# Kernel tuning notes

Measured on AMD Instinct MI355X. Metric: run time of the kernel, lower is better.

## Reference

```python
import jax, jax.numpy as jnp
import numpy as np

N_NODES = 50000
N_EDGES = 800000
IN_F = 512
H_F = 32
HEADS = 8
N_CLS = 40
NEG_SLOPE = 0.2


def gat_conv(h, W, al, ar, b, src, dst, n_heads, d_out):
    """DGL-style GATConv. h: [N, F_in]; W: [F_in, n_heads*d_out];
    al, ar: [n_heads, d_out]; b: [n_heads*d_out]. Returns [N, n_heads, d_out]."""
    n = h.shape[0]
    feat = (h @ W).reshape(n, n_heads, d_out)            # [N, H, D]
    el = jnp.sum(feat * al[None], axis=-1)               # [N, H]
    er = jnp.sum(feat * ar[None], axis=-1)               # [N, H]
    e = jax.nn.leaky_relu(el[src] + er[dst], NEG_SLOPE)  # [E, H]
    # numerically stable edge softmax per destination node
    m = jax.ops.segment_max(e, dst, num_segments=n)      # [N, H]
    m = jnp.where(jnp.isfinite(m), m, 0.0)
    ee = jnp.exp(e - m[dst])                             # [E, H]
    den = jax.ops.segment_sum(ee, dst, num_segments=n)   # [N, H]
    alpha = ee / jnp.maximum(den[dst], 1e-9)             # [E, H]
    msg = alpha[:, :, None] * feat[src]                  # [E, H, D]
    rst = jax.ops.segment_sum(msg, dst, num_segments=n)  # [N, H, D]
    return rst + b.reshape(1, n_heads, d_out)


def setup_inputs() -> dict:
    key = jax.random.key(0)
    ks = jax.random.split(key, 16)
    hid = H_F * HEADS
    s = lambda fan: 1.0 / np.sqrt(fan)
    return {
        "in_feat": jax.random.normal(ks[0], (N_NODES, IN_F), jnp.float32),
        "src": jax.random.randint(ks[1], (N_EDGES,), 0, N_NODES, jnp.int32),
        "dst": jax.random.randint(ks[2], (N_EDGES,), 0, N_NODES, jnp.int32),
        "W0": jax.random.normal(ks[3], (IN_F, hid), jnp.float32) * s(IN_F),
        "al0": jax.random.normal(ks[4], (HEADS, H_F), jnp.float32) * s(H_F),
        "ar0": jax.random.normal(ks[5], (HEADS, H_F), jnp.float32) * s(H_F),
        "b0": jnp.zeros((hid,), jnp.float32),
        "W1": jax.random.normal(ks[6], (hid, hid), jnp.float32) * s(hid),
        "al1": jax.random.normal(ks[7], (HEADS, H_F), jnp.float32) * s(H_F),
        "ar1": jax.random.normal(ks[8], (HEADS, H_F), jnp.float32) * s(H_F),
        "b1": jnp.zeros((hid,), jnp.float32),
        "W2": jax.random.normal(ks[9], (hid, N_CLS), jnp.float32) * s(hid),
        "al2": jax.random.normal(ks[10], (1, N_CLS), jnp.float32) * s(N_CLS),
        "ar2": jax.random.normal(ks[11], (1, N_CLS), jnp.float32) * s(N_CLS),
        "b2": jnp.zeros((N_CLS,), jnp.float32),
    }


def reference(in_feat, src, dst, W0, al0, ar0, b0, W1, al1, ar1, b1,
              W2, al2, ar2, b2):
    n = in_feat.shape[0]
    # layer 0 + ReLU (dropout p=0.0 is identity) + flatten heads
    h = gat_conv(in_feat, W0, al0, ar0, b0, src, dst, HEADS, H_F)
    h = jax.nn.relu(h).reshape(n, -1)
    # layer 1
    h = gat_conv(h, W1, al1, ar1, b1, src, dst, HEADS, H_F)
    h = jax.nn.relu(h).reshape(n, -1)
    # output layer, single head, no activation
    h = gat_conv(h, W2, al2, ar2, b2, src, dst, 1, N_CLS)
    return h.reshape(n, -1)
```

## Files before the change

kernel.cpp:

```cpp
#include <hip/hip_runtime.h>
#include <hip/hip_bf16.h>

#define N_NODES 50000
#define N_EDGES 800000
#define IN_F 512
#define HID 256
#define HEADS 8
#define DHEAD 32
#define N_CLS 40
#define NCLS_PAD 64

typedef __bf16 bf16x8 __attribute__((ext_vector_type(8)));
typedef float f32x4 __attribute__((ext_vector_type(4)));
typedef float f32x2 __attribute__((ext_vector_type(2)));

#define AT_AL0 0
#define AT_AR0 256
#define AT_AL1 512
#define AT_AR1 768
#define AT_AL2 1024
#define AT_AR2 1088
#define AT_B0  1152
#define AT_B1  1408
#define AT_B2  1664
#define AT_SZ  1792

__device__ __forceinline__ float ldflag(const void* p, long long i, int isbf) {
  return isbf ? __bfloat162float(((const __hip_bfloat16*)p)[i])
              : ((const float*)p)[i];
}
__device__ __forceinline__ float blo(unsigned u) { return __uint_as_float(u << 16); }
__device__ __forceinline__ float bhi(unsigned u) { return __uint_as_float(u & 0xffff0000u); }
__device__ __forceinline__ f32x2 bpair(unsigned u) {
  f32x2 r;
  r.x = __uint_as_float(u << 16);
  r.y = __uint_as_float(u & 0xffff0000u);
  return r;
}
__device__ __forceinline__ unsigned pk2(float a, float b) {
  unsigned x = __bfloat16_as_ushort(__float2bfloat16(a));
  unsigned y = __bfloat16_as_ushort(__float2bfloat16(b));
  return x | (y << 16);
}
__device__ __forceinline__ void gload16(const unsigned short* g, unsigned short* l) {
  __builtin_amdgcn_global_load_lds((__attribute__((address_space(1))) void*)g,
                                   (__attribute__((address_space(3))) void*)l, 16, 0, 0);
}

__global__ void k_detect_prep(const unsigned short* __restrict__ raw, int* __restrict__ flag,
                              const void* al0, const void* ar0, const void* al1, const void* ar1,
                              const void* al2, const void* ar2, const void* b0, const void* b1,
                              const void* b2, float* __restrict__ att, int* __restrict__ cursor) {
  __shared__ int cnt[256];
  int t = threadIdx.x;
  for (int i = t; i < N_NODES; i += 256) cursor[i] = 0;
  int c = 0;
  for (int i = t; i < 8192; i += 256) {
    int e = (raw[i] >> 7) & 0xFF;
    if (e >= 0x90) c++;
  }
  cnt[t] = c;
  __syncthreads();
  for (int s = 128; s; s >>= 1) {
    if (t < s) cnt[t] += cnt[t + s];
    __syncthreads();
  }
  __shared__ int sflag;
  if (t == 0) { sflag = (cnt[0] > 64) ? 0 : 1; *flag = sflag; }
  __syncthreads();
  int isbf = sflag;
  att[AT_AL0 + t] = ldflag(al0, t, isbf);
  att[AT_AR0 + t] = ldflag(ar0, t, isbf);
  att[AT_AL1 + t] = ldflag(al1, t, isbf);
  att[AT_AR1 + t] = ldflag(ar1, t, isbf);
  att[AT_B0 + t]  = ldflag(b0, t, isbf);
  att[AT_B1 + t]  = ldflag(b1, t, isbf);
  if (t < N_CLS) {
    att[AT_AL2 + t] = ldflag(al2, t, isbf);
    att[AT_AR2 + t] = ldflag(ar2, t, isbf);
    att[AT_B2 + t]  = ldflag(b2, t, isbf);
  }
}

__global__ void k_hist(const int* __restrict__ dst, int* __restrict__ cnt) {
  int e = blockIdx.x * blockDim.x + threadIdx.x;
  if (e < N_EDGES) atomicAdd(&cnt[dst[e]], 1);
}

#define SCAN_B 512
#define SCAN_NB ((N_NODES + SCAN_B - 1) / SCAN_B)

__global__ __launch_bounds__(SCAN_B) void k_scan_blocks(const int* __restrict__ deg,
                                                        int* __restrict__ excl,
                                                        int* __restrict__ partial) {
  __shared__ int buf[SCAN_B];
  int t = threadIdx.x;
  int i = blockIdx.x * SCAN_B + t;
  int v = (i < N_NODES) ? deg[i] : 0;
  buf[t] = v;
  __syncthreads();
  for (int off = 1; off < SCAN_B; off <<= 1) {
    int x = (t >= off) ? buf[t - off] : 0;
    __syncthreads();
    buf[t] += x;
    __syncthreads();
  }
  if (i < N_NODES) excl[i] = buf[t] - v;
  if (t == SCAN_B - 1) partial[blockIdx.x] = buf[t];
}

__global__ void k_scan_partials(int* __restrict__ partial, int* __restrict__ rowptr) {
  __shared__ int buf[SCAN_NB];
  int t = threadIdx.x;
  if (t < SCAN_NB) buf[t] = partial[t];
  __syncthreads();
  if (t == 0) {
    int run = 0;
    for (int b = 0; b < SCAN_NB; b++) { int v = buf[b]; buf[b] = run; run += v; }
    rowptr[N_NODES] = run;
  }
  __syncthreads();
  if (t < SCAN_NB) partial[t] = buf[t];
}

__global__ void k_scan_add(int* __restrict__ rowptr, const int* __restrict__ partial,
                           int* __restrict__ cursor) {
  int i = blockIdx.x * blockDim.x + threadIdx.x;
  if (i < N_NODES) {
    rowptr[i] += partial[i / SCAN_B];
    cursor[i] = 0;
  }
}

__global__ void k_scatter(const int* __restrict__ src, const int* __restrict__ dst,
                          const int* __restrict__ rowptr, int* __restrict__ cursor,
                          int* __restrict__ csr_src) {
  int e = blockIdx.x * blockDim.x + threadIdx.x;
  if (e < N_EDGES) {
    int d = dst[e];
    int pos = rowptr[d] + atomicAdd(&cursor[d], 1);
    csr_src[pos] = src[e];
  }
}

#define TW0 (HID * IN_F)
#define TW1 (TW0 + HID * HID)
#define TW2 (TW1 + NCLS_PAD * HID)
__global__ void k_transpose_all(const void* __restrict__ W0, const void* __restrict__ W1,
                                const void* __restrict__ W2,
                                __hip_bfloat16* __restrict__ w0t, __hip_bfloat16* __restrict__ w1t,
                                __hip_bfloat16* __restrict__ w2t, const int* __restrict__ flag) {
  int isbf = *flag;
  int i = blockIdx.x * blockDim.x + threadIdx.x;
  if (i < TW0) {
    int n = i >> 9, k = i & 511;
    w0t[i] = __float2bfloat16(ldflag(W0, (long long)k * HID + n, isbf));
  } else if (i < TW1) {
    int j = i - TW0;
    int n = j >> 8, k = j & 255;
    w1t[j] = __float2bfloat16(ldflag(W1, (long long)k * HID + n, isbf));
  } else if (i < TW2) {
    int j = i - TW1;
    int n = j >> 8, k = j & 255;
    float v = (n < N_CLS) ? ldflag(W2, (long long)k * N_CLS + n, isbf) : 0.f;
    w2t[j] = __float2bfloat16(v);
  }
}

__device__ __forceinline__ uint4 loadA(const void* A, int isbf, int ga, int M, int K, int off) {
  uint4 av = make_uint4(0u, 0u, 0u, 0u);
  if (ga < M) {
    if (isbf) {
      av = *(const uint4*)((const __hip_bfloat16*)A + (size_t)ga * K + off);
    } else {
      const float* ap = (const float*)A + (size_t)ga * K + off;
      float4 f1 = *(const float4*)ap;
      float4 f2 = *(const float4*)(ap + 4);
      av.x = pk2(f1.x, f1.y); av.y = pk2(f1.z, f1.w);
      av.z = pk2(f2.x, f2.y); av.w = pk2(f2.z, f2.w);
    }
  }
  return av;
}

__global__ __launch_bounds__(256) void k_gemm128(const void* __restrict__ A,
                                                 const __hip_bfloat16* __restrict__ Bt,
                                                 __hip_bfloat16* __restrict__ C,
                                                 int M, int K, int N,
                                                 const int* __restrict__ flag, int force_bf,
                                                 const float* __restrict__ al,
                                                 const float* __restrict__ ar,
                                                 float* __restrict__ el,
                                                 float* __restrict__ er, int fuse_eler) {
  __shared__ unsigned short sA[128 * 32];
  __shared__ unsigned short sB[128 * 32];
  const int isbf = force_bf ? 1 : *flag;
  int nwg = gridDim.x;
  int q = nwg >> 3, r = nwg & 7;
  int xcd = blockIdx.x & 7, lid = blockIdx.x >> 3;
  int logical = (xcd < r ? xcd * (q + 1) : r * (q + 1) + (xcd - r) * q) + lid;
  int nblk = N >> 7;
  int mb = logical / nblk;
  int nb = logical - mb * nblk;
  int m0 = mb * 128, n0 = nb * 128;
  int tid = threadIdx.x;
  int wave = tid >> 6, lane = tid & 63;
  int wm = (wave >> 1) * 64, wn = (wave & 1) * 64;
  int lm = lane & 15, quad = lane >> 4;
  int c0 = (wave << 7) + lane, c1 = c0 + 64;
  int rA0 = c0 >> 2, rA1 = c1 >> 2;
  int col0 = (c0 & 3) << 3, col1 = (c1 & 3) << 3;
  int gr0 = m0 + rA0; if (gr0 > M - 1) gr0 = M - 1;
  int gr1 = m0 + rA1; if (gr1 > M - 1) gr1 = M - 1;
  const unsigned short* Ab = (const unsigned short*)A;
  const float* Af = (const float*)A;
  const unsigned short* Bb = (const unsigned short*)Bt;
  size_t aog0 = (size_t)gr0 * K + col0;
  size_t aog1 = (size_t)gr1 * K + col1;
  size_t bog0 = (size_t)(n0 + rA0) * K + col0;
  size_t bog1 = (size_t)(n0 + rA1) * K + col1;
  unsigned short* la0 = &sA[c0 << 3];
  unsigned short* la1 = &sA[c1 << 3];
  unsigned short* lb0 = &sB[c0 << 3];
  unsigned short* lb1 = &sB[c1 << 3];
  const char* sAb = (const char*)sA;
  const char* sBb = (const char*)sB;
  int fq = quad << 4;
  int aoff[4], boff[4];
  #pragma unroll
  for (int i = 0; i < 4; i++) {
    aoff[i] = ((wm + i * 16 + lm) << 6) + fq;
    boff[i] = ((wn + i * 16 + lm) << 6) + fq;
  }
  f32x4 acc[4][4] = {};
  for (int k0 = 0; k0 < K; k0 += 32) {
    __syncthreads();
    if (isbf) {
      gload16(Ab + aog0 + k0, la0);
      gload16(Ab + aog1 + k0, la1);
    } else {
      const float* p0 = Af + aog0 + k0;
      const float* p1 = Af + aog1 + k0;
      float4 x0 = *(const float4*)p0, y0 = *(const float4*)(p0 + 4);
      float4 x1 = *(const float4*)p1, y1 = *(const float4*)(p1 + 4);
      *(uint4*)la0 = make_uint4(pk2(x0.x, x0.y), pk2(x0.z, x0.w), pk2(y0.x, y0.y), pk2(y0.z, y0.w));
      *(uint4*)la1 = make_uint4(pk2(x1.x, x1.y), pk2(x1.z, x1.w), pk2(y1.x, y1.y), pk2(y1.z, y1.w));
    }
    gload16(Bb + bog0 + k0, lb0);
    gload16(Bb + bog1 + k0, lb1);
    __syncthreads();
    bf16x8 af[4], bfr[4];
    #pragma unroll
    for (int i = 0; i < 4; i++) {
      af[i]  = *(const bf16x8*)(sAb + aoff[i]);
      bfr[i] = *(const bf16x8*)(sBb + boff[i]);
    }
    #pragma unroll
    for (int mi = 0; mi < 4; mi++)
      #pragma unroll
      for (int ni = 0; ni < 4; ni++)
        acc[mi][ni] = __builtin_amdgcn_mfma_f32_16x16x32_bf16(af[mi], bfr[ni], acc[mi][ni], 0, 0, 0);
  }
  #pragma unroll
  for (int mi = 0; mi < 4; mi++) {
    #pragma unroll
    for (int r2 = 0; r2 < 4; r2++) {
      int gm = m0 + wm + mi * 16 + (quad << 2) + r2;
      if (gm < M) {
        #pragma unroll
        for (int ni = 0; ni < 4; ni++) {
          int gn = n0 + wn + ni * 16 + lm;
          C[(size_t)gm * N + gn] = __float2bfloat16(acc[mi][ni][r2]);
        }
      }
    }
  }
  if (fuse_eler) {
    int h0 = (n0 + wn) >> 5;
    float ala[4], ara[4];
    #pragma unroll
    for (int ni = 0; ni < 4; ni++) {
      int idx = (h0 + (ni >> 1)) * DHEAD + ((ni & 1) << 4) + lm;
      ala[ni] = al[idx];
      ara[ni] = ar[idx];
    }
    #pragma unroll
    for (int mi = 0; mi < 4; mi++)
      #pragma unroll
      for (int r2 = 0; r2 < 4; r2++) {
        int gm = m0 + wm + mi * 16 + (quad << 2) + r2;
        #pragma unroll
        for (int hp = 0; hp < 2; hp++) {
          float pl = acc[mi][2 * hp][r2] * ala[2 * hp] + acc[mi][2 * hp + 1][r2] * ala[2 * hp + 1];
          float pr = acc[mi][2 * hp][r2] * ara[2 * hp] + acc[mi][2 * hp + 1][r2] * ara[2 * hp + 1];
          #pragma unroll
          for (int d = 1; d < 16; d <<= 1) {
            pl += __shfl_xor(pl, d, 16);
            pr += __shfl_xor(pr, d, 16);
          }
          if (lm == 0 && gm < M) {
            el[gm * HEADS + h0 + hp] = pl;
            er[gm * HEADS + h0 + hp] = pr;
          }
        }
      }
  }
}

__global__ __launch_bounds__(256) void k_gemm64(const void* __restrict__ A,
                                                const __hip_bfloat16* __restrict__ Bt,
                                                __hip_bfloat16* __restrict__ C,
                                                int M, int K, int N,
                                                const int* __restrict__ flag, int force_bf,
                                                const float* __restrict__ al,
                                                const float* __restrict__ ar,
                                                float* __restrict__ el,
                                                float* __restrict__ er, int fuse_eler) {
  __shared__ unsigned short As[64][40];
  __shared__ unsigned short Bs[64][40];
  const int isbf = force_bf ? 1 : *flag;
  int nblk = N >> 6;
  int per = nblk << 3;
  int g = blockIdx.x / per;
  int i2 = blockIdx.x - g * per;
  int mb = g * 8 + (i2 & 7);
  int nb = i2 >> 3;
  int m0 = mb * 64, n0 = nb * 64;
  if (m0 >= M) return;
  int tid = threadIdx.x;
  int lrow = tid >> 2;
  int lcol = (tid & 3) * 8;
  int wave = tid >> 6, lane = tid & 63;
  int wm = (wave >> 1) * 32, wn = (wave & 1) * 32;
  int lm = lane & 15, quad = lane >> 4;
  f32x4 acc[2][2] = {};
  uint4 av = loadA(A, isbf, m0 + lrow, M, K, lcol);
  uint4 bv = *(const uint4*)(Bt + (size_t)(n0 + lrow) * K + lcol);
  for (int k0 = 0; k0 < K; k0 += 32) {
    __syncthreads();
    *(uint4*)(&As[lrow][lcol]) = av;
    *(uint4*)(&Bs[lrow][lcol]) = bv;
    __syncthreads();
    uint4 avn = make_uint4(0u, 0u, 0u, 0u), bvn = make_uint4(0u, 0u, 0u, 0u);
    if (k0 + 32 < K) {
      avn = loadA(A, isbf, m0 + lrow, M, K, k0 + 32 + lcol);
      bvn = *(const uint4*)(Bt + (size_t)(n0 + lrow) * K + k0 + 32 + lcol);
    }
    bf16x8 af[2], bfr[2];
    #pragma unroll
    for (int i = 0; i < 2; i++) {
      af[i]  = *(const bf16x8*)(&As[wm + i * 16 + lm][quad * 8]);
      bfr[i] = *(const bf16x8*)(&Bs[wn + i * 16 + lm][quad * 8]);
    }
    #pragma unroll
    for (int mi = 0; mi < 2; mi++)
      #pragma unroll
      for (int ni = 0; ni < 2; ni++)
        acc[mi][ni] = __builtin_amdgcn_mfma_f32_16x16x32_bf16(af[mi], bfr[ni], acc[mi][ni], 0, 0, 0);
    av = avn; bv = bvn;
  }
  #pragma unroll
  for (int mi = 0; mi < 2; mi++)
    #pragma unroll
    for (int ni = 0; ni < 2; ni++)
      #pragma unroll
      for (int r = 0; r < 4; r++) {
        int gm = m0 + wm + mi * 16 + quad * 4 + r;
        int gn = n0 + wn + ni * 16 + lm;
        if (gm < M) C[(size_t)gm * N + gn] = __float2bfloat16(acc[mi][ni][r]);
      }
  if (fuse_eler) {
    int hg = (n0 + wn) >> 5;
    float ala[2], ara[2];
    #pragma unroll
    for (int ni = 0; ni < 2; ni++) {
      ala[ni] = al[hg * DHEAD + ni * 16 + lm];
      ara[ni] = ar[hg * DHEAD + ni * 16 + lm];
    }
    #pragma unroll
    for (int mi = 0; mi < 2; mi++)
      #pragma unroll
      for (int r = 0; r < 4; r++) {
        float pl = acc[mi][0][r] * ala[0] + acc[mi][1][r] * ala[1];
        float pr = acc[mi][0][r] * ara[0] + acc[mi][1][r] * ara[1];
        #pragma unroll
        for (int d = 1; d < 16; d <<= 1) {
          pl += __shfl_xor(pl, d, 16);
          pr += __shfl_xor(pr, d, 16);
        }
        int gm = m0 + wm + mi * 16 + quad * 4 + r;
        if (lm == 0 && gm < M) {
          el[gm * HEADS + hg] = pl;
          er[gm * HEADS + hg] = pr;
        }
      }
  }
}

__global__ void k_eler2(const __hip_bfloat16* __restrict__ feat2,
                        const float* __restrict__ al, const float* __restrict__ ar,
                        float* __restrict__ el, float* __restrict__ er) {
  int n = blockIdx.x * blockDim.x + threadIdx.x;
  if (n >= N_NODES) return;
  const __hip_bfloat16* f = feat2 + (size_t)n * NCLS_PAD;
  float sl = 0.f, sr = 0.f;
  for (int d = 0; d < N_CLS; d++) {
    float v = __bfloat162float(f[d]);
    sl += v * al[d];
    sr += v * ar[d];
  }
  el[n] = sl;
  er[n] = sr;
}

__global__ __launch_bounds__(256) void k_aggregate8(const int* __restrict__ rowptr,
                                                    const int* __restrict__ csr_src,
                                                    const uint4* __restrict__ feat_rows,
                                                    const float* __restrict__ el,
                                                    const float* __restrict__ er,
                                                    const float* __restrict__ bias,
                                                    __hip_bfloat16* __restrict__ out) {
  __shared__ float lds_acc[8][256];
  __shared__ float lds_l[8][32];
  int n = blockIdx.x;
  int t = threadIdx.x;
  int slot = t >> 5;
  int c = t & 31;
  int hh = c >> 2;
  float er_n = er[n * HEADS + hh];
  int beg = rowptr[n], end = rowptr[n + 1];
  float l = 0.f;
  f32x2 a0 = {0.f, 0.f}, a1 = {0.f, 0.f}, a2 = {0.f, 0.f}, a3 = {0.f, 0.f};
  const char* fb = (const char*)feat_rows;
  unsigned cb = (unsigned)c << 4;
  int i = beg + slot;
  for (; i + 8 < end; i += 16) {
    int s1 = csr_src[i];
    int s2 = csr_src[i + 8];
    float el1 = el[s1 * HEADS + hh];
    float el2 = el[s2 * HEADS + hh];
    uint4 f1 = *(const uint4*)(fb + (((unsigned)s1 << 9) | cb));
    uint4 f2 = *(const uint4*)(fb + (((unsigned)s2 << 9) | cb));
    float x1 = el1 + er_n, x2 = el2 + er_n;
    float e1 = x1 > 0.f ? x1 : 0.2f * x1;
    float e2 = x2 > 0.f ? x2 : 0.2f * x2;
    float p1 = __expf(fminf(e1, 60.f));
    float p2 = __expf(fminf(e2, 60.f));
    l += p1 + p2;
    a0 += bpair(f1.x) * p1; a1 += bpair(f1.y) * p1;
    a2 += bpair(f1.z) * p1; a3 += bpair(f1.w) * p1;
    a0 += bpair(f2.x) * p2; a1 += bpair(f2.y) * p2;
    a2 += bpair(f2.z) * p2; a3 += bpair(f2.w) * p2;
  }
  if (i < end) {
    int s = csr_src[i];
    float elv = el[s * HEADS + hh];
    uint4 fv = *(const uint4*)(fb + (((unsigned)s << 9) | cb));
    float x = elv + er_n;
    float e = x > 0.f ? x : 0.2f * x;
    float p = __expf(fminf(e, 60.f));
    l += p;
    a0 += bpair(fv.x) * p; a1 += bpair(fv.y) * p;
    a2 += bpair(fv.z) * p; a3 += bpair(fv.w) * p;
  }
  *(float4*)&lds_acc[slot][c * 8]     = make_float4(a0.x, a0.y, a1.x, a1.y);
  *(float4*)&lds_acc[slot][c * 8 + 4] = make_float4(a2.x, a2.y, a3.x, a3.y);
  lds_l[slot][c] = l;
  __syncthreads();
  float a = 0.f, L = 0.f;
  #pragma unroll
  for (int s2 = 0; s2 < 8; s2++) { a += lds_acc[s2][t]; L += lds_l[s2][t >> 3]; }
  float o = a / fmaxf(L, 1e-9f) + bias[t];
  o = fmaxf(o, 0.f);
  out[(size_t)n * HID + t] = __float2bfloat16(o);
}

__global__ __launch_bounds__(256) void k_aggregate1(const int* __restrict__ rowptr,
                                                    const int* __restrict__ csr_src,
                                                    const uint4* __restrict__ fr2,
                                                    const float* __restrict__ el,
                                                    const float* __restrict__ er,
                                                    const float* __restrict__ bias,
                                                    void* __restrict__ out,
                                                    const int* __restrict__ flag) {
  __shared__ float lds_acc[32][64];
  __shared__ float lds_l[32][8];
  int isbf = *flag;
  int n = blockIdx.x;
  int t = threadIdx.x;
  int slot = t >> 3;
  int c = t & 7;
  float er_n = er[n];
  int beg = rowptr[n], end = rowptr[n + 1];
  float l = 0.f;
  f32x2 a0 = {0.f, 0.f}, a1 = {0.f, 0.f}, a2 = {0.f, 0.f}, a3 = {0.f, 0.f};
  const char* fb = (const char*)fr2;
  unsigned cb = (unsigned)c << 4;
  int i = beg + slot;
  for (; i + 32 < end; i += 64) {
    int s1 = csr_src[i], s2 = csr_src[i + 32];
    float el1 = el[s1], el2 = el[s2];
    uint4 f1 = *(const uint4*)(fb + (((unsigned)s1 << 7) | cb));
    uint4 f2 = *(const uint4*)(fb + (((unsigned)s2 << 7) | cb));
    float x1 = el1 + er_n, x2 = el2 + er_n;
    float e1 = x1 > 0.f ? x1 : 0.2f * x1;
    float e2 = x2 > 0.f ? x2 : 0.2f * x2;
    float p1 = __expf(fminf(e1, 60.f));
    float p2 = __expf(fminf(e2, 60.f));
    l += p1 + p2;
    a0 += bpair(f1.x) * p1; a1 += bpair(f1.y) * p1;
    a2 += bpair(f1.z) * p1; a3 += bpair(f1.w) * p1;
    a0 += bpair(f2.x) * p2; a1 += bpair(f2.y) * p2;
    a2 += bpair(f2.z) * p2; a3 += bpair(f2.w) * p2;
  }
  if (i < end) {
    int s = csr_src[i];
    float x = el[s] + er_n;
    uint4 fv = *(const uint4*)(fb + (((unsigned)s << 7) | cb));
    float e = x > 0.f ? x : 0.2f * x;
    float p = __expf(fminf(e, 60.f));
    l += p;
    a0 += bpair(fv.x) * p; a1 += bpair(fv.y) * p;
    a2 += bpair(fv.z) * p; a3 += bpair(fv.w) * p;
  }
  *(float4*)&lds_acc[slot][c * 8]     = make_float4(a0.x, a0.y, a1.x, a1.y);
  *(float4*)&lds_acc[slot][c * 8 + 4] = make_float4(a2.x, a2.y, a3.x, a3.y);
  lds_l[slot][c] = l;
  __syncthreads();
  if (t < N_CLS) {
    float a = 0.f, L = 0.f;
    #pragma unroll
    for (int s2 = 0; s2 < 32; s2++) { a += lds_acc[s2][t]; L += lds_l[s2][t >> 3]; }
    float o = a / fmaxf(L, 1e-9f) + bias[t];
    if (isbf) ((__hip_bfloat16*)out)[(size_t)n * N_CLS + t] = __float2bfloat16(o);
    else      ((float*)out)[(size_t)n * N_CLS + t] = o;
  }
}

static inline size_t align_up(size_t x) { return (x + 255) & ~(size_t)255; }

extern "C" void kernel_launch(void* const* d_in, const int* in_sizes, int n_in,
                              void* d_out, int out_size, void* d_ws, size_t ws_size,
                              hipStream_t stream) {
  const void* in_feat = d_in[0];
  const int* src = (const int*)d_in[1];
  const int* dst = (const int*)d_in[2];
  const void* W0  = d_in[3];
  const void* al0 = d_in[4];
  const void* ar0 = d_in[5];
  const void* b0  = d_in[6];
  const void* W1  = d_in[7];
  const void* al1 = d_in[8];
  const void* ar1 = d_in[9];
  const void* b1  = d_in[10];
  const void* W2  = d_in[11];
  const void* al2 = d_in[12];
  const void* ar2 = d_in[13];
  const void* b2  = d_in[14];

  char* p = (char*)d_ws;
  int* flag = (int*)p;                   p += 256;
  float* att = (float*)p;                p += align_up(AT_SZ * sizeof(float));
  int* rowptr = (int*)p;                 p += align_up((N_NODES + 1) * sizeof(int));
  int* cursor = (int*)p;                 p += align_up(N_NODES * sizeof(int));
  int* csr_src = (int*)p;                p += align_up(N_EDGES * sizeof(int));
  int* partial = (int*)p;                p += align_up(SCAN_NB * sizeof(int));
  __hip_bfloat16* feat16 = (__hip_bfloat16*)p; p += align_up((size_t)N_NODES * HID * sizeof(__hip_bfloat16));
  __hip_bfloat16* h16 = (__hip_bfloat16*)p;    p += align_up((size_t)N_NODES * HID * sizeof(__hip_bfloat16));
  float* el = (float*)p;                 p += align_up((size_t)N_NODES * HEADS * sizeof(float));
  float* er = (float*)p;                 p += align_up((size_t)N_NODES * HEADS * sizeof(float));
  __hip_bfloat16* w0t = (__hip_bfloat16*)p;    p += align_up((size_t)HID * IN_F * sizeof(__hip_bfloat16));
  __hip_bfloat16* w1t = (__hip_bfloat16*)p;    p += align_up((size_t)HID * HID * sizeof(__hip_bfloat16));
  __hip_bfloat16* w2t = (__hip_bfloat16*)p;    p += align_up((size_t)NCLS_PAD * HID * sizeof(__hip_bfloat16));

  const int EB = (N_EDGES + 255) / 256;
  const int MB64 = (N_NODES + 63) / 64;
  const int GROUPS = (MB64 + 7) / 8;
  const int G1 = GROUPS * 8 * 1;
  const int MB128 = (N_NODES + 127) / 128;
  const int GX = MB128 * 2;

  k_detect_prep<<<1, 256, 0, stream>>>((const unsigned short*)in_feat, flag,
                                       al0, ar0, al1, ar1, al2, ar2, b0, b1, b2, att, cursor);

  k_hist<<<EB, 256, 0, stream>>>(dst, cursor);
  k_scan_blocks<<<SCAN_NB, SCAN_B, 0, stream>>>(cursor, rowptr, partial);
  k_scan_partials<<<1, 128, 0, stream>>>(partial, rowptr);
  k_scan_add<<<(N_NODES + 255) / 256, 256, 0, stream>>>(rowptr, partial, cursor);
  k_scatter<<<EB, 256, 0, stream>>>(src, dst, rowptr, cursor, csr_src);

  k_transpose_all<<<(TW2 + 255) / 256, 256, 0, stream>>>(W0, W1, W2, w0t, w1t, w2t, flag);

  k_gemm128<<<GX, 256, 0, stream>>>(in_feat, w0t, feat16, N_NODES, IN_F, HID, flag, 0,
                                    att + AT_AL0, att + AT_AR0, el, er, 1);
  k_aggregate8<<<N_NODES, 256, 0, stream>>>(rowptr, csr_src, (const uint4*)feat16, el, er, att + AT_B0, h16);

  k_gemm128<<<GX, 256, 0, stream>>>(h16, w1t, feat16, N_NODES, HID, HID, flag, 1,
                                    att + AT_AL1, att + AT_AR1, el, er, 1);
  k_aggregate8<<<N_NODES, 256, 0, stream>>>(rowptr, csr_src, (const uint4*)feat16, el, er, att + AT_B1, h16);

  k_gemm64<<<G1, 256, 0, stream>>>(h16, w2t, feat16, N_NODES, HID, NCLS_PAD, flag, 1,
                                   nullptr, nullptr, nullptr, nullptr, 0);
  k_eler2<<<(N_NODES + 255) / 256, 256, 0, stream>>>(feat16, att + AT_AL2, att + AT_AR2, el, er);
  k_aggregate1<<<N_NODES, 256, 0, stream>>>(rowptr, csr_src, (const uint4*)feat16, el, er, att + AT_B2, d_out, flag);
}
```

Before: 554.5 us.

## Triple-buffer GEMM shared-memory tiles with async prefetch two tiles ahead

The 128x128 bf16 MFMA GEMM now keeps three LDS buffers for A and B and issues global-to-LDS loads for tile t+2 while computing on tile t. Explicit vmcnt waits, a single barrier per iteration and sched_barriers replace the two __syncthreads per k-step. The aim is to hide global load latency behind MFMA work. The cost is triple the LDS footprint (48KB), which may reduce occupancy. Correctness relies on the hand-written waitcnt counts.

```diff
diff --git a/kernel.cpp b/kernel.cpp
--- a/kernel.cpp
+++ b/kernel.cpp
@@ -192,8 +192,8 @@
                                                  const float* __restrict__ ar,
                                                  float* __restrict__ el,
                                                  float* __restrict__ er, int fuse_eler) {
-  __shared__ unsigned short sA[128 * 32];
-  __shared__ unsigned short sB[128 * 32];
+  __shared__ unsigned short sA[3][128 * 32];
+  __shared__ unsigned short sB[3][128 * 32];
   const int isbf = force_bf ? 1 : *flag;
   int nwg = gridDim.x;
   int q = nwg >> 3, r = nwg & 7;
@@ -219,12 +219,7 @@
   size_t aog1 = (size_t)gr1 * K + col1;
   size_t bog0 = (size_t)(n0 + rA0) * K + col0;
   size_t bog1 = (size_t)(n0 + rA1) * K + col1;
-  unsigned short* la0 = &sA[c0 << 3];
-  unsigned short* la1 = &sA[c1 << 3];
-  unsigned short* lb0 = &sB[c0 << 3];
-  unsigned short* lb1 = &sB[c1 << 3];
-  const char* sAb = (const char*)sA;
-  const char* sBb = (const char*)sB;
+  int lo0 = c0 << 3, lo1 = c1 << 3;
   int fq = quad << 4;
   int aoff[4], boff[4];
   #pragma unroll
@@ -233,22 +228,48 @@
     boff[i] = ((wn + i * 16 + lm) << 6) + fq;
   }
   f32x4 acc[4][4] = {};
-  for (int k0 = 0; k0 < K; k0 += 32) {
-    __syncthreads();
+  int nk = K >> 5;
+
+  #define STAGE_TILE(j, b)                                                              \
+    do {                                                                                \
+      size_t ko = (size_t)(j) << 5;                                                     \
+      if (isbf) {                                                                       \
+        gload16(Ab + aog0 + ko, &sA[(b)][lo0]);                                         \
+        gload16(Ab + aog1 + ko, &sA[(b)][lo1]);                                         \
+        gload16(Bb + bog0 + ko, &sB[(b)][lo0]);                                         \
+        gload16(Bb + bog1 + ko, &sB[(b)][lo1]);                                         \
+      } else {                                                                          \
+        gload16(Bb + bog0 + ko, &sB[(b)][lo0]);                                         \
+        gload16(Bb + bog1 + ko, &sB[(b)][lo1]);                                         \
+        const float* p0 = Af + aog0 + ko;                                               \
+        const float* p1 = Af + aog1 + ko;                                               \
+        float4 x0 = *(const float4*)p0, y0 = *(const float4*)(p0 + 4);                  \
+        float4 x1 = *(const float4*)p1, y1 = *(const float4*)(p1 + 4);                  \
+        *(uint4*)&sA[(b)][lo0] =                                                        \
+            make_uint4(pk2(x0.x, x0.y), pk2(x0.z, x0.w), pk2(y0.x, y0.y), pk2(y0.z, y0.w)); \
+        *(uint4*)&sA[(b)][lo1] =                                                        \
+            make_uint4(pk2(x1.x, x1.y), pk2(x1.z, x1.w), pk2(y1.x, y1.y), pk2(y1.z, y1.w)); \
+        asm volatile("s_waitcnt lgkmcnt(0)" ::: "memory");                              \
+      }                                                                                 \
+    } while (0)
+
+  STAGE_TILE(0, 0);
+  if (nk > 1) STAGE_TILE(1, 1);
+  int bufT = 0;
+  int bufP = 2;
+  for (int t = 0; t < nk; ++t) {
     if (isbf) {
-      gload16(Ab + aog0 + k0, la0);
-      gload16(Ab + aog1 + k0, la1);
+      if (t + 1 < nk) asm volatile("s_waitcnt vmcnt(4)" ::: "memory");
+      else            asm volatile("s_waitcnt vmcnt(0)" ::: "memory");
     } else {
-      const float* p0 = Af + aog0 + k0;
-      const float* p1 = Af + aog1 + k0;
-      float4 x0 = *(const float4*)p0, y0 = *(const float4*)(p0 + 4);
-      float4 x1 = *(const float4*)p1, y1 = *(const float4*)(p1 + 4);
-      *(uint4*)la0 = make_uint4(pk2(x0.x, x0.y), pk2(x0.z, x0.w), pk2(y0.x, y0.y), pk2(y0.z, y0.w));
-      *(uint4*)la1 = make_uint4(pk2(x1.x, x1.y), pk2(x1.z, x1.w), pk2(y1.x, y1.y), pk2(y1.z, y1.w));
-    }
-    gload16(Bb + bog0 + k0, lb0);
-    gload16(Bb + bog1 + k0, lb1);
-    __syncthreads();
+      asm volatile("s_waitcnt vmcnt(0)" ::: "memory");
+    }
+    __builtin_amdgcn_s_barrier();
+    __builtin_amdgcn_sched_barrier(0);
+    if (t + 2 < nk) STAGE_TILE(t + 2, bufP);
+    __builtin_amdgcn_sched_barrier(0);
+    const char* sAb = (const char*)&sA[bufT][0];
+    const char* sBb = (const char*)&sB[bufT][0];
     bf16x8 af[4], bfr[4];
     #pragma unroll
     for (int i = 0; i < 4; i++) {
@@ -260,7 +281,11 @@
       #pragma unroll
       for (int ni = 0; ni < 4; ni++)
         acc[mi][ni] = __builtin_amdgcn_mfma_f32_16x16x32_bf16(af[mi], bfr[ni], acc[mi][ni], 0, 0, 0);
-  }
+    __builtin_amdgcn_sched_barrier(0);
+    bufT = (bufT == 2) ? 0 : bufT + 1;
+    bufP = (bufP == 2) ? 0 : bufP + 1;
+  }
+  #undef STAGE_TILE
   #pragma unroll
   for (int mi = 0; mi < 4; mi++) {
     #pragma unroll
```

Result: no change. 550.0 us (-0.8%).
